# Performance work log

Hardware: AMD Instinct MI355X
Metric: run time of the kernel (lower is better)

Reference implementation:

```python
import jax, jax.numpy as jnp
import numpy as np

N_NODES = 50000
N_EDGES = 1_600_000
D_IN = 128
D_OUT = 128


def setup_inputs() -> dict:
    key = jax.random.key(0)
    k1, k2, k3, k4 = jax.random.split(key, 4)
    x = jax.random.normal(k1, (N_NODES, D_IN), dtype=jnp.float32)
    weight = jax.random.normal(k2, (D_IN, D_OUT), dtype=jnp.float32)
    bias = jnp.zeros((D_OUT,), dtype=jnp.float32)
    edge_row = jax.random.randint(k3, (N_EDGES,), 0, N_NODES, dtype=jnp.int64 if jax.config.jax_enable_x64 else jnp.int32)
    edge_col = jax.random.randint(k4, (N_EDGES,), 0, N_NODES, dtype=jnp.int64 if jax.config.jax_enable_x64 else jnp.int32)
    return {"x": x, "weight": weight, "bias": bias, "edge_row": edge_row, "edge_col": edge_col}


def reference(x, weight, bias, edge_row, edge_col):
    # edges_sparse is a binary [N, N] COO adjacency; edge (row=i, col=j) has value 1.
    n = x.shape[0]
    ones = jnp.ones(edge_row.shape[0], dtype=x.dtype)
    # out_degree = A.sum(dim=1): row sums of the adjacency
    out_degree = jax.ops.segment_sum(ones, edge_row, num_segments=n)
    deg_inv_sqrt = out_degree ** -0.5  # D = diag(deg^-0.5)
    # (D A D) x  ==  scatter_i sum_j deg_i^-0.5 * deg_j^-0.5 * x_j over edges (i, j)
    w = deg_inv_sqrt[edge_row] * deg_inv_sqrt[edge_col]  # [E]
    msg = w[:, None] * x[edge_col]                        # [E, D_IN]
    agg = jax.ops.segment_sum(msg, edge_row, num_segments=n)  # [N, D_IN]
    # dense projection + bias
    return agg @ weight + bias
```

## Files before the change

kernel.cpp:

```cpp
#include <hip/hip_runtime.h>
#include <hip/hip_bf16.h>

#define NODES   50000
#define EDGES   1600000
#define DIM     128
#define NB      391
#define BSTRIDE 4608
#define TILE    8192
#define EPT     32
#define NTILES  196
#define ZROW    50000

typedef unsigned int   u32;
typedef unsigned short u16;
typedef __attribute__((ext_vector_type(4))) float f32x4;
typedef __attribute__((ext_vector_type(8))) short s16x8;

__device__ inline u16 f2bf(float f) {
  __hip_bfloat16 h = __float2bfloat16(f);
  return *reinterpret_cast<u16*>(&h);
}

__global__ __launch_bounds__(256) void k_prep(const float* __restrict__ W,
                                              u16* __restrict__ wts,
                                              int* __restrict__ gcursor) {
  __shared__ float T[32 * 132];
  int t = threadIdx.x;
  int gi = blockIdx.x * 256 + t;
  if (gi < NB) gcursor[gi] = gi * BSTRIDE;
  int c0 = blockIdx.x * 32;
#pragma unroll
  for (int i = 0; i < 16; ++i) {
    int idx = i * 256 + t;
    int k = idx >> 5;
    int cc = idx & 31;
    T[cc * 132 + k] = W[k * 128 + c0 + cc];
  }
  __syncthreads();
#pragma unroll
  for (int i = 0; i < 2; ++i) {
    int idx = i * 256 + t;
    int cc = idx >> 4;
    int kc = idx & 15;
    int c = c0 + cc;
    int kbase = kc * 8;
    u32 p[4];
#pragma unroll
    for (int u = 0; u < 4; ++u) {
      float a = T[cc * 132 + kbase + 2 * u];
      float b = T[cc * 132 + kbase + 2 * u + 1];
      p[u] = (u32)f2bf(a) | ((u32)f2bf(b) << 16);
    }
    int off = c * 256 + ((kbase * 2) ^ ((c & 15) << 4));
    *(uint4*)((char*)wts + off) = make_uint4(p[0], p[1], p[2], p[3]);
  }
}

__global__ __launch_bounds__(256) void k_binA(const int* __restrict__ erow,
                                              const int* __restrict__ ecol,
                                              int* __restrict__ gcursor,
                                              u32* __restrict__ binned) {
  __shared__ int hist[NB];
  __shared__ int lcur[NB];
  int t = threadIdx.x;
  for (int b = t; b < NB; b += 256) hist[b] = 0;
  __syncthreads();
  int base = blockIdx.x * TILE;
  u32 v[EPT];
#pragma unroll
  for (int k = 0; k < 8; ++k) {
    int e4 = base + k * 1024 + t * 4;
    if (e4 < EDGES) {
      int4 rr = *(const int4*)&erow[e4];
      int4 cc = *(const int4*)&ecol[e4];
      v[k * 4 + 0] = ((u32)rr.x << 16) | (u32)cc.x;
      v[k * 4 + 1] = ((u32)rr.y << 16) | (u32)cc.y;
      v[k * 4 + 2] = ((u32)rr.z << 16) | (u32)cc.z;
      v[k * 4 + 3] = ((u32)rr.w << 16) | (u32)cc.w;
      atomicAdd(&hist[(u32)rr.x >> 7], 1);
      atomicAdd(&hist[(u32)rr.y >> 7], 1);
      atomicAdd(&hist[(u32)rr.z >> 7], 1);
      atomicAdd(&hist[(u32)rr.w >> 7], 1);
    } else {
      v[k * 4 + 0] = 0xffffffffu;
      v[k * 4 + 1] = 0xffffffffu;
      v[k * 4 + 2] = 0xffffffffu;
      v[k * 4 + 3] = 0xffffffffu;
    }
  }
  __syncthreads();
  for (int b = t; b < NB; b += 256) {
    int h = hist[b];
    lcur[b] = h ? atomicAdd(&gcursor[b], h) : 0;
  }
  __syncthreads();
#pragma unroll
  for (int k = 0; k < EPT; ++k) {
    if (v[k] != 0xffffffffu) {
      int b = (int)(v[k] >> 23);
      int pos = atomicAdd(&lcur[b], 1);
      if (pos < (b + 1) * BSTRIDE) binned[pos] = v[k];
    }
  }
}

__global__ __launch_bounds__(256) void k_binB(const u32* __restrict__ binned,
                                              const int* __restrict__ gcur,
                                              int* __restrict__ rpS,
                                              int* __restrict__ rpE,
                                              float* __restrict__ dis,
                                              u16* __restrict__ cols) {
  __shared__ int cnt[128];
  __shared__ int sc[128];
  __shared__ int lcur[128];
  int b = blockIdx.x;
  int t = threadIdx.x;
  int n0 = b << 7;
  int s = b * BSTRIDE;
  int e = gcur[b];
  if (e > s + BSTRIDE) e = s + BSTRIDE;
  if (t < 128) cnt[t] = 0;
  __syncthreads();
  for (int j = s + t; j < e; j += 256) {
    u32 v = binned[j];
    atomicAdd(&cnt[(int)(v >> 16) - n0], 1);
  }
  __syncthreads();
  if (t < 128) sc[t] = cnt[t];
  __syncthreads();
  for (int off = 1; off < 128; off <<= 1) {
    int tmp = (t >= off && t < 128) ? sc[t - off] : 0;
    __syncthreads();
    if (t < 128) sc[t] += tmp;
    __syncthreads();
  }
  if (t < 128) {
    int n = n0 + t;
    if (n < NODES) {
      int excl = s + sc[t] - cnt[t];
      rpS[n] = excl;
      rpE[n] = excl + cnt[t];
      lcur[t] = excl;
      dis[n] = rsqrtf((float)cnt[t]);
    }
  }
  __syncthreads();
  for (int j = s + t; j < e; j += 256) {
    u32 v = binned[j];
    int local = (int)(v >> 16) - n0;
    int pos = atomicAdd(&lcur[local], 1);
    cols[pos] = (u16)(v & 0xffffu);
  }
}

__global__ __launch_bounds__(256) void k_gemm(const float* __restrict__ x,
                                              const u16* __restrict__ wts,
                                              const float* __restrict__ dis,
                                              u16* __restrict__ y2) {
  __shared__ u16 xs[64 * 128];
  __shared__ u16 ws[128 * 128];
  const int t = threadIdx.x;
  const int bb = blockIdx.x * 64;

  {
    const uint4* src = (const uint4*)wts;
    uint4* dst = (uint4*)ws;
#pragma unroll
    for (int i = 0; i < 8; ++i) dst[i * 256 + t] = src[i * 256 + t];
  }
  {
#pragma unroll
    for (int i = 0; i < 8; ++i) {
      int goff = i * 4096 + t * 16;
      int row = goff >> 9;
      int gr = bb + row;
      float4 v = make_float4(0.f, 0.f, 0.f, 0.f);
      if (gr < NODES) v = *(const float4*)((const char*)x + (size_t)gr * 512 + (goff & 511));
      u32 lo = (u32)f2bf(v.x) | ((u32)f2bf(v.y) << 16);
      u32 hi = (u32)f2bf(v.z) | ((u32)f2bf(v.w) << 16);
      int colb = (goff & 511) >> 1;
      int off = row * 256 + (colb ^ ((row & 15) << 4));
      *(uint2*)((char*)xs + off) = make_uint2(lo, hi);
    }
  }
  __syncthreads();

  const int w = t >> 6, l = t & 63, m = l & 15, g = l >> 4;
  f32x4 acc[8];
#pragma unroll
  for (int j = 0; j < 8; ++j) acc[j] = (f32x4)0.0f;

  const char* xb = (const char*)xs;
  const char* wb = (const char*)ws;
  const int arow = w * 16 + m;
#pragma unroll
  for (int s = 0; s < 4; ++s) {
    int kx = (g * 16 + s * 64) ^ (m << 4);
    s16x8 a = *(const s16x8*)(xb + arow * 256 + kx);
#pragma unroll
    for (int j = 0; j < 8; ++j) {
      s16x8 b = *(const s16x8*)(wb + (j * 16 + m) * 256 + kx);
      acc[j] = __builtin_amdgcn_mfma_f32_16x16x32_bf16(a, b, acc[j], 0, 0, 0);
    }
  }

  int rbase = bb + w * 16 + g * 4;
  float4 d4 = *(const float4*)&dis[rbase];
#pragma unroll
  for (int j = 0; j < 8; ++j) {
#pragma unroll
    for (int r = 0; r < 4; ++r) {
      int gr = rbase + r;
      float dv = (r == 0) ? d4.x : (r == 1) ? d4.y : (r == 2) ? d4.z : d4.w;
      float val = (gr < NODES) ? acc[j][r] * dv : 0.0f;
      y2[(size_t)gr * 128 + j * 16 + m] = f2bf(val);
    }
  }
}

__global__ __launch_bounds__(256) void k_agg(const u16* __restrict__ y2,
                                             const int* __restrict__ rpS,
                                             const int* __restrict__ rpE,
                                             const u16* __restrict__ cols,
                                             const float* __restrict__ dis,
                                             const float* __restrict__ bias,
                                             float* __restrict__ out) {
  int node = (blockIdx.x * 256 + threadIdx.x) >> 6;
  int l = threadIdx.x & 63;
  if (node >= NODES) return;
  int q = l >> 4;
  int m = l & 15;
  int s = rpS[node];
  int e = rpE[node];

  float a0 = 0.f, a1 = 0.f, a2 = 0.f, a3 = 0.f;
  float a4 = 0.f, a5 = 0.f, a6 = 0.f, a7 = 0.f;
  const uint4* yb = (const uint4*)y2;

  int c0 = (s + q      < e) ? (int)cols[s + q]      : ZROW;
  int c1 = (s + q + 4  < e) ? (int)cols[s + q + 4]  : ZROW;
  int c2 = (s + q + 8  < e) ? (int)cols[s + q + 8]  : ZROW;
  int c3 = (s + q + 12 < e) ? (int)cols[s + q + 12] : ZROW;
  int c4 = (s + q + 16 < e) ? (int)cols[s + q + 16] : ZROW;
  int c5 = (s + q + 20 < e) ? (int)cols[s + q + 20] : ZROW;
  int c6 = (s + q + 24 < e) ? (int)cols[s + q + 24] : ZROW;
  int c7 = (s + q + 28 < e) ? (int)cols[s + q + 28] : ZROW;

  for (int jb = s; jb < e; jb += 32) {
    int nb = jb + 32;
    int d0 = (nb + q      < e) ? (int)cols[nb + q]      : ZROW;
    int d1 = (nb + q + 4  < e) ? (int)cols[nb + q + 4]  : ZROW;
    int d2 = (nb + q + 8  < e) ? (int)cols[nb + q + 8]  : ZROW;
    int d3 = (nb + q + 12 < e) ? (int)cols[nb + q + 12] : ZROW;
    int d4 = (nb + q + 16 < e) ? (int)cols[nb + q + 16] : ZROW;
    int d5 = (nb + q + 20 < e) ? (int)cols[nb + q + 20] : ZROW;
    int d6 = (nb + q + 24 < e) ? (int)cols[nb + q + 24] : ZROW;
    int d7 = (nb + q + 28 < e) ? (int)cols[nb + q + 28] : ZROW;
    uint4 v0 = yb[c0 * 16 + m];
    uint4 v1 = yb[c1 * 16 + m];
    uint4 v2 = yb[c2 * 16 + m];
    uint4 v3 = yb[c3 * 16 + m];
    uint4 v4 = yb[c4 * 16 + m];
    uint4 v5 = yb[c5 * 16 + m];
    uint4 v6 = yb[c6 * 16 + m];
    uint4 v7 = yb[c7 * 16 + m];
#define ACC(v)                                   \
    a0 += __uint_as_float((v).x << 16);          \
    a1 += __uint_as_float((v).x & 0xffff0000u);  \
    a2 += __uint_as_float((v).y << 16);          \
    a3 += __uint_as_float((v).y & 0xffff0000u);  \
    a4 += __uint_as_float((v).z << 16);          \
    a5 += __uint_as_float((v).z & 0xffff0000u);  \
    a6 += __uint_as_float((v).w << 16);          \
    a7 += __uint_as_float((v).w & 0xffff0000u);
    ACC(v0) ACC(v1) ACC(v2) ACC(v3) ACC(v4) ACC(v5) ACC(v6) ACC(v7)
#undef ACC
    c0 = d0; c1 = d1; c2 = d2; c3 = d3;
    c4 = d4; c5 = d5; c6 = d6; c7 = d7;
  }

  a0 += __shfl_xor(a0, 16); a0 += __shfl_xor(a0, 32);
  a1 += __shfl_xor(a1, 16); a1 += __shfl_xor(a1, 32);
  a2 += __shfl_xor(a2, 16); a2 += __shfl_xor(a2, 32);
  a3 += __shfl_xor(a3, 16); a3 += __shfl_xor(a3, 32);
  a4 += __shfl_xor(a4, 16); a4 += __shfl_xor(a4, 32);
  a5 += __shfl_xor(a5, 16); a5 += __shfl_xor(a5, 32);
  a6 += __shfl_xor(a6, 16); a6 += __shfl_xor(a6, 32);
  a7 += __shfl_xor(a7, 16); a7 += __shfl_xor(a7, 32);

  float di = (e > s) ? dis[node] : 0.0f;
  if (q < 2) {
    float r0 = q ? a4 : a0;
    float r1 = q ? a5 : a1;
    float r2 = q ? a6 : a2;
    float r3 = q ? a7 : a3;
    float4 bb = *(const float4*)&bias[m * 8 + q * 4];
    f32x4 o;
    o[0] = bb.x + di * r0;
    o[1] = bb.y + di * r1;
    o[2] = bb.z + di * r2;
    o[3] = bb.w + di * r3;
    __builtin_nontemporal_store(o, (f32x4*)&out[(size_t)node * 128 + m * 8 + q * 4]);
  }
}

extern "C" void kernel_launch(void* const* d_in, const int* in_sizes, int n_in,
                              void* d_out, int out_size, void* d_ws, size_t ws_size,
                              hipStream_t stream) {
  const float* x    = (const float*)d_in[0];
  const float* W    = (const float*)d_in[1];
  const float* bias = (const float*)d_in[2];
  const int*   erow = (const int*)d_in[3];
  const int*   ecol = (const int*)d_in[4];
  float* out = (float*)d_out;

  char* ws = (char*)d_ws;
  int*   gcursor = (int*)(ws + 0);
  int*   rpS     = (int*)(ws + 4096);
  int*   rpE     = (int*)(ws + 208896);
  float* dis     = (float*)(ws + 409600);
  u16*   wts     = (u16*)(ws + 614400);
  u32*   binned  = (u32*)(ws + 655360);
  u16*   cols    = (u16*)(ws + 7864320);
  u16*   y2      = (u16*)(ws + 11468800);

  k_prep<<<4, 256, 0, stream>>>(W, wts, gcursor);
  k_binA<<<NTILES, 256, 0, stream>>>(erow, ecol, gcursor, binned);
  k_binB<<<NB, 256, 0, stream>>>(binned, gcursor, rpS, rpE, dis, cols);
  k_gemm<<<(NODES + 63) / 64, 256, 0, stream>>>(x, wts, dis, y2);
  k_agg<<<(NODES * 64 + 255) / 256, 256, 0, stream>>>(y2, rpS, rpE, cols, dis, bias, out);
}
```

Measured before the change: 98.09 us.

## Stage bin columns in LDS, pack row pointers, shuffle-distribute column indices

k_binB keeps its binned entries in registers so the bin is read from global memory once instead of twice. It scatters column indices into an LDS staging buffer and then writes them to global memory with coalesced 32-bit stores. Row start and end pointers are packed into a single int2 array, so k_agg needs one load per node for them. k_agg now fetches each 32-column chunk with one 32-bit load per lane and hands indices out with cross-lane shuffles, instead of eight scattered 16-bit loads per lane. In exchange it adds shuffle and branch overhead and special-case handling for odd start offsets.

```diff
diff --git a/kernel.cpp b/kernel.cpp
--- a/kernel.cpp
+++ b/kernel.cpp
@@ -106,24 +106,29 @@
 
 __global__ __launch_bounds__(256) void k_binB(const u32* __restrict__ binned,
                                               const int* __restrict__ gcur,
-                                              int* __restrict__ rpS,
-                                              int* __restrict__ rpE,
+                                              int2* __restrict__ rp2,
                                               float* __restrict__ dis,
                                               u16* __restrict__ cols) {
   __shared__ int cnt[128];
   __shared__ int sc[128];
   __shared__ int lcur[128];
+  __shared__ u16 stage[BSTRIDE];
   int b = blockIdx.x;
   int t = threadIdx.x;
   int n0 = b << 7;
   int s = b * BSTRIDE;
   int e = gcur[b];
   if (e > s + BSTRIDE) e = s + BSTRIDE;
+  int cntE = e - s;
   if (t < 128) cnt[t] = 0;
   __syncthreads();
-  for (int j = s + t; j < e; j += 256) {
-    u32 v = binned[j];
-    atomicAdd(&cnt[(int)(v >> 16) - n0], 1);
+  u32 held[18];
+#pragma unroll
+  for (int k = 0; k < 18; ++k) {
+    int j = s + t + k * 256;
+    u32 v = (j < e) ? binned[j] : 0xffffffffu;
+    held[k] = v;
+    if (v != 0xffffffffu) atomicAdd(&cnt[(int)(v >> 16) - n0], 1);
   }
   __syncthreads();
   if (t < 128) sc[t] = cnt[t];
@@ -137,19 +142,27 @@
   if (t < 128) {
     int n = n0 + t;
     if (n < NODES) {
-      int excl = s + sc[t] - cnt[t];
-      rpS[n] = excl;
-      rpE[n] = excl + cnt[t];
-      lcur[t] = excl;
+      int lexcl = sc[t] - cnt[t];
+      rp2[n] = make_int2(s + lexcl, s + lexcl + cnt[t]);
+      lcur[t] = lexcl;
       dis[n] = rsqrtf((float)cnt[t]);
     }
   }
   __syncthreads();
-  for (int j = s + t; j < e; j += 256) {
-    u32 v = binned[j];
-    int local = (int)(v >> 16) - n0;
-    int pos = atomicAdd(&lcur[local], 1);
-    cols[pos] = (u16)(v & 0xffffu);
+#pragma unroll
+  for (int k = 0; k < 18; ++k) {
+    u32 v = held[k];
+    if (v != 0xffffffffu) {
+      int pos = atomicAdd(&lcur[(int)(v >> 16) - n0], 1);
+      stage[pos] = (u16)(v & 0xffffu);
+    }
+  }
+  __syncthreads();
+  {
+    u32* dst = (u32*)(cols + s);
+    const u32* src = (const u32*)stage;
+    int nw = (cntE + 1) >> 1;
+    for (int i = t; i < nw; i += 256) dst[i] = src[i];
   }
 }
 
@@ -219,8 +232,7 @@
 }
 
 __global__ __launch_bounds__(256) void k_agg(const u16* __restrict__ y2,
-                                             const int* __restrict__ rpS,
-                                             const int* __restrict__ rpE,
+                                             const int2* __restrict__ rp2,
                                              const u16* __restrict__ cols,
                                              const float* __restrict__ dis,
                                              const float* __restrict__ bias,
@@ -230,32 +242,63 @@
   if (node >= NODES) return;
   int q = l >> 4;
   int m = l & 15;
-  int s = rpS[node];
-  int e = rpE[node];
+  int2 rr = rp2[node];
+  int s = rr.x;
+  int e = rr.y;
 
   float a0 = 0.f, a1 = 0.f, a2 = 0.f, a3 = 0.f;
   float a4 = 0.f, a5 = 0.f, a6 = 0.f, a7 = 0.f;
   const uint4* yb = (const uint4*)y2;
-
-  int c0 = (s + q      < e) ? (int)cols[s + q]      : ZROW;
-  int c1 = (s + q + 4  < e) ? (int)cols[s + q + 4]  : ZROW;
-  int c2 = (s + q + 8  < e) ? (int)cols[s + q + 8]  : ZROW;
-  int c3 = (s + q + 12 < e) ? (int)cols[s + q + 12] : ZROW;
-  int c4 = (s + q + 16 < e) ? (int)cols[s + q + 16] : ZROW;
-  int c5 = (s + q + 20 < e) ? (int)cols[s + q + 20] : ZROW;
-  int c6 = (s + q + 24 < e) ? (int)cols[s + q + 24] : ZROW;
-  int c7 = (s + q + 28 < e) ? (int)cols[s + q + 28] : ZROW;
+  const u32* cols32 = (const u32*)cols;
+  const int hi = q & 1;
+  const int wbase = q >> 1;
+
+  u32 w0 = cols32[(s >> 1) + m];
+  int odd = s & 1;
+
+#define COLAT(base, kk)                       \
+    (((base) + q + 4 * (kk) < e)                                                        \
+       ? ((odd ? ((((base) + q + 4 * (kk)) & 1)                                         \
+                    ? (__shfl(w0_cur, ((((base) + q + 4 * (kk)) - b0) >> 1)) & 0xffffu) \
+                    : (__shfl(w0_cur, ((((base) + q + 4 * (kk)) - b0) >> 1)) >> 16))    \
+                : 0)) : 0)
+
+  int c0, c1, c2, c3, c4, c5, c6, c7;
+  {
+    int b0 = (s >> 1) * 2;
+#define GETC(kk, dst)  {                                                        \
+      int idx = s + q + 4 * (kk);                                               \
+      if (idx < e) {                                                            \
+        int rel = idx - b0;                            \
+        u32 wv = __shfl(w0, rel >> 1);                                          \
+        dst = (rel & 1) ? (int)(wv >> 16) : (int)(wv & 0xffffu);                \
+      } else dst = ZROW; }
+    GETC(0, c0) GETC(1, c1) GETC(2, c2) GETC(3, c3)
+    GETC(4, c4) GETC(5, c5) GETC(6, c6) GETC(7, c7)
+#undef GETC
+    if (odd) {
+      if (q == 3) { int idx = s + q + 28; c7 = (idx < e) ? (int)cols[idx] : ZROW; }
+    }
+  }
 
   for (int jb = s; jb < e; jb += 32) {
     int nb = jb + 32;
-    int d0 = (nb + q      < e) ? (int)cols[nb + q]      : ZROW;
-    int d1 = (nb + q + 4  < e) ? (int)cols[nb + q + 4]  : ZROW;
-    int d2 = (nb + q + 8  < e) ? (int)cols[nb + q + 8]  : ZROW;
-    int d3 = (nb + q + 12 < e) ? (int)cols[nb + q + 12] : ZROW;
-    int d4 = (nb + q + 16 < e) ? (int)cols[nb + q + 16] : ZROW;
-    int d5 = (nb + q + 20 < e) ? (int)cols[nb + q + 20] : ZROW;
-    int d6 = (nb + q + 24 < e) ? (int)cols[nb + q + 24] : ZROW;
-    int d7 = (nb + q + 28 < e) ? (int)cols[nb + q + 28] : ZROW;
+    u32 wn = cols32[(nb >> 1) + m];
+    int d0, d1, d2, d3, d4x, d5, d6, d7;
+    {
+      int b0 = (nb >> 1) * 2;
+#define GETC(kk, dst)  {                                                        \
+      int idx = nb + q + 4 * (kk);                                              \
+      if (idx < e) {                                                            \
+        int rel = idx - b0;                                                     \
+        u32 wv = __shfl(wn, rel >> 1);                                          \
+        dst = (rel & 1) ? (int)(wv >> 16) : (int)(wv & 0xffffu);                \
+      } else dst = ZROW; }
+      GETC(0, d0) GETC(1, d1) GETC(2, d2) GETC(3, d3)
+      GETC(4, d4x) GETC(5, d5) GETC(6, d6) GETC(7, d7)
+#undef GETC
+      if (odd && q == 3) { int idx = nb + 31; d7 = (idx < e) ? (int)cols[idx] : ZROW; }
+    }
     uint4 v0 = yb[c0 * 16 + m];
     uint4 v1 = yb[c1 * 16 + m];
     uint4 v2 = yb[c2 * 16 + m];
@@ -276,7 +319,8 @@
     ACC(v0) ACC(v1) ACC(v2) ACC(v3) ACC(v4) ACC(v5) ACC(v6) ACC(v7)
 #undef ACC
     c0 = d0; c1 = d1; c2 = d2; c3 = d3;
-    c4 = d4; c5 = d5; c6 = d6; c7 = d7;
+    c4 = d4x; c5 = d5; c6 = d6; c7 = d7;
+    w0 = wn;
   }
 
   a0 += __shfl_xor(a0, 16); a0 += __shfl_xor(a0, 32);
@@ -316,8 +360,7 @@
 
   char* ws = (char*)d_ws;
   int*   gcursor = (int*)(ws + 0);
-  int*   rpS     = (int*)(ws + 4096);
-  int*   rpE     = (int*)(ws + 208896);
+  int2*  rp2     = (int2*)(ws + 4096);
   float* dis     = (float*)(ws + 409600);
   u16*   wts     = (u16*)(ws + 614400);
   u32*   binned  = (u32*)(ws + 655360);
@@ -326,7 +369,7 @@
 
   k_prep<<<4, 256, 0, stream>>>(W, wts, gcursor);
   k_binA<<<NTILES, 256, 0, stream>>>(erow, ecol, gcursor, binned);
-  k_binB<<<NB, 256, 0, stream>>>(binned, gcursor, rpS, rpE, dis, cols);
+  k_binB<<<NB, 256, 0, stream>>>(binned, gcursor, rp2, dis, cols);
   k_gemm<<<(NODES + 63) / 64, 256, 0, stream>>>(x, wts, dis, y2);
-  k_agg<<<(NODES * 64 + 255) / 256, 256, 0, stream>>>(y2, rpS, rpE, cols, dis, bias, out);
-}
+  k_agg<<<(NODES * 64 + 255) / 256, 256, 0, stream>>>(y2, rp2, cols, dis, bias, out);
+}
```

Measured after the change: 101.1 us. 1.03x slower.
